# Kernel optimization log

Measured on AMD Instinct MI355X. Metric: run time of the kernel, lower is better.

Reference implementation:

```python
import jax, jax.numpy as jnp
import numpy as np

B, A, C, H, W = 8, 9, 21, 100, 100
M = 32
N = A * H * W
POS_THR, NEG_THR = 0.25, 0.1


def setup_inputs() -> dict:
    key = jax.random.key(0)
    k1, k2, k3, k4, k5, k6, k7 = jax.random.split(key, 7)
    cls_output = jax.random.normal(k1, (B, A, C, H, W), jnp.float32)
    reg_output = jax.random.normal(k2, (B, A, 4, H, W), jnp.float32) * 0.1
    # valid xyxy anchors: centers in [32,480], sizes in [16,128]
    ctr = jax.random.uniform(k3, (N, 2), minval=32.0, maxval=480.0)
    wh = jax.random.uniform(k4, (N, 2), minval=16.0, maxval=128.0)
    anchors = jnp.concatenate([ctr - wh / 2, ctr + wh / 2], axis=1)
    tctr = jax.random.uniform(k5, (B, M, 2), minval=32.0, maxval=480.0)
    twh = jax.random.uniform(k6, (B, M, 2), minval=16.0, maxval=128.0)
    target_boxes = jnp.concatenate([tctr - twh / 2, tctr + twh / 2], axis=2)
    target_labels = jax.random.randint(k7, (B, M), 1, C)
    return dict(cls_output=cls_output, reg_output=reg_output, anchors=anchors,
                target_boxes=target_boxes, target_labels=target_labels)


def _decode_boxes(reg, anchors):
    # inverse of the encode math in the loss: tx=(t*2-1), ctr=a_ctr+tx*aw/4, w=aw*exp(tw)
    aw = anchors[:, 2] - anchors[:, 0]
    ah = anchors[:, 3] - anchors[:, 1]
    acx = anchors[:, 0] + 0.5 * aw
    acy = anchors[:, 1] + 0.5 * ah
    tx = reg[:, 0] * 2.0 - 1.0
    ty = reg[:, 1] * 2.0 - 1.0
    cx = acx + tx * aw / 4.0
    cy = acy + ty * ah / 4.0
    w = aw * jnp.exp(reg[:, 2])
    h = ah * jnp.exp(reg[:, 3])
    return jnp.stack([cx - w / 2, cy - h / 2, cx + w / 2, cy + h / 2], axis=1)


def _pairwise_iou(a, b):  # a: [N,4], b: [M,4] xyxy
    lt = jnp.maximum(a[:, None, :2], b[None, :, :2])  # [N,M,2]
    rb = jnp.minimum(a[:, None, 2:], b[None, :, 2:])
    wh = jnp.clip(rb - lt, 0.0)
    inter = wh[..., 0] * wh[..., 1]
    area_a = (a[:, 2] - a[:, 0]) * (a[:, 3] - a[:, 1])
    area_b = (b[:, 2] - b[:, 0]) * (b[:, 3] - b[:, 1])
    union = area_a[:, None] + area_b[None, :] - inter
    return inter / jnp.maximum(union, 1e-8)


def _smooth_l1(d):
    ad = jnp.abs(d)
    return jnp.where(ad < 1.0, 0.5 * d * d, ad - 0.5)


def _per_image(cls_i, reg_i, anchors, boxes, labels):
    # [A,4,H,W] -> [4,A,H,W] -> [4,N] -> [N,4]; same for cls
    reg_flat = jnp.transpose(reg_i, (1, 0, 2, 3)).reshape(4, -1).T
    cls_flat = jnp.transpose(cls_i, (1, 0, 2, 3)).reshape(C, -1).T  # [N,C]
    decoded = _decode_boxes(reg_flat, anchors)
    ious = _pairwise_iou(decoded, boxes)  # [N,M]
    max_iou = ious.max(axis=1)
    max_idx = ious.argmax(axis=1)
    pos = max_iou >= POS_THR
    neg = max_iou < NEG_THR
    n_pos = pos.sum()
    n_neg = neg.sum()
    posf = pos.astype(cls_flat.dtype)
    negf = neg.astype(cls_flat.dtype)

    lse = jax.nn.logsumexp(cls_flat, axis=1)  # [N]
    matched_labels = labels[max_idx]  # [N]
    ce_pos = lse - jnp.take_along_axis(cls_flat, matched_labels[:, None], axis=1)[:, 0]
    ce_neg = lse - cls_flat[:, 0]
    cls_loss = (ce_pos * posf).sum() / jnp.maximum(n_pos, 1).astype(cls_flat.dtype)
    cls_loss = cls_loss + (ce_neg * negf).sum() / jnp.maximum(n_neg, 1).astype(cls_flat.dtype)

    # encode gt against anchors (vectorized over all N, masked to positives)
    aw = anchors[:, 2] - anchors[:, 0]
    ah = anchors[:, 3] - anchors[:, 1]
    acx = anchors[:, 0] + 0.5 * aw
    acy = anchors[:, 1] + 0.5 * ah
    gb = boxes[max_idx]  # [N,4]
    gw = gb[:, 2] - gb[:, 0]
    gh = gb[:, 3] - gb[:, 1]
    gcx = gb[:, 0] + 0.5 * gw
    gcy = gb[:, 1] + 0.5 * gh
    tx = ((gcx - acx) * (4.0 / aw) + 1.0) / 2.0
    ty = ((gcy - acy) * (4.0 / ah) + 1.0) / 2.0
    tw = jnp.log(gw / aw)
    th = jnp.log(gh / ah)
    reg_targets = jnp.stack([tx, ty, tw, th], axis=1)  # [N,4]
    sl1 = _smooth_l1(reg_flat - reg_targets)
    reg_loss = (sl1 * posf[:, None]).sum() / jnp.maximum(n_pos * 4, 1).astype(cls_flat.dtype)
    return cls_loss, reg_loss, n_pos


def reference(cls_output, reg_output, anchors, target_boxes, target_labels):
    cls_losses, reg_losses, n_pos = jax.vmap(
        _per_image, in_axes=(0, 0, None, 0, 0))(cls_output, reg_output, anchors,
                                                 target_boxes, target_labels)
    total_pos = n_pos.sum()
    cls_final = cls_losses.mean()
    reg_final = reg_losses.sum() / jnp.maximum(total_pos, 1).astype(cls_losses.dtype)
    total = cls_final + reg_final
    return total, cls_final, reg_final, total_pos
```

## Files before the change

### kernel.cpp

```cpp
#include <hip/hip_runtime.h>

#define HWSZ   10000
#define A_     9
#define C_     21
#define B_     8
#define M_     32
#define TPB    256
#define Q_     2500
#define SUBS   10
#define BPI    (A_*SUBS)
#define P_     (B_*BPI)

__device__ __forceinline__ float smooth_l1(float d) {
    float ad = fabsf(d);
    return ad < 1.f ? 0.5f * d * d : ad - 0.5f;
}

__device__ __forceinline__ float wave_red(float v) {
    #pragma unroll
    for (int o = 32; o; o >>= 1) v += __shfl_down(v, o);
    return v;
}

__device__ __forceinline__ float fc(const float4& v, int k) {
    return k == 0 ? v.x : k == 1 ? v.y : k == 2 ? v.z : v.w;
}

__device__ __forceinline__ void det_body(
    const float* __restrict__ cls, const float* __restrict__ reg,
    const float* __restrict__ anchors,
    const float4* sbox, const float* sarea, const int* slbl,
    int b, int a, int q,
    float& ce_pos, float& ce_neg, float& sl1, float& nposf, float& nnegf)
{
    float4 an[4], rg[4];
    const float4* anch4 = (const float4*)anchors + (size_t)a * HWSZ + q * 4;
    #pragma unroll
    for (int k = 0; k < 4; ++k) an[k] = anch4[k];
    const float4* reg4 = (const float4*)reg + ((b * A_ + a) * 4) * Q_ + q;
    #pragma unroll
    for (int k = 0; k < 4; ++k) rg[k] = reg4[k * Q_];
    const float4* cls4 = (const float4*)cls + ((b * A_ + a) * C_) * Q_ + q;
    float4 bufA[10];
    #pragma unroll
    for (int j = 0; j < 10; ++j) bufA[j] = cls4[j * Q_];

    float aw[4], ah[4], acx[4], acy[4];
    float r0[4], r1[4], r2[4], r3[4];
    float dx1[4], dy1[4], dx2[4], dy2[4], ara[4];
    #pragma unroll
    for (int k = 0; k < 4; ++k) {
        float4 A = an[k];
        aw[k] = A.z - A.x; ah[k] = A.w - A.y;
        acx[k] = A.x + 0.5f * aw[k]; acy[k] = A.y + 0.5f * ah[k];
        r0[k] = fc(rg[0], k); r1[k] = fc(rg[1], k);
        r2[k] = fc(rg[2], k); r3[k] = fc(rg[3], k);
        float tx = r0[k] * 2.f - 1.f, ty = r1[k] * 2.f - 1.f;
        float cx = acx[k] + tx * aw[k] * 0.25f;
        float cy = acy[k] + ty * ah[k] * 0.25f;
        float w = aw[k] * __expf(r2[k]), h = ah[k] * __expf(r3[k]);
        dx1[k] = cx - 0.5f * w; dy1[k] = cy - 0.5f * h;
        dx2[k] = cx + 0.5f * w; dy2[k] = cy + 0.5f * h;
        ara[k] = w * h;
    }

    float bi[4] = {-1.f, -1.f, -1.f, -1.f};
    float bu[4] = { 1.f,  1.f,  1.f,  1.f};
    int   bx_[4] = {0, 0, 0, 0};
    #pragma unroll 4
    for (int m = 0; m < M_; ++m) {
        float4 gb = sbox[m];
        float  am = sarea[m];
        #pragma unroll
        for (int k = 0; k < 4; ++k) {
            float lx = fmaxf(dx1[k], gb.x), ly = fmaxf(dy1[k], gb.y);
            float rx = fminf(dx2[k], gb.z), ry = fminf(dy2[k], gb.w);
            float iw = fmaxf(rx - lx, 0.f), ih = fmaxf(ry - ly, 0.f);
            float inter = iw * ih;
            float uni   = ara[k] + am - inter;
            bool  gt    = inter * bu[k] > bi[k] * uni;
            bi[k]  = gt ? inter : bi[k];
            bu[k]  = gt ? uni   : bu[k];
            bx_[k] = gt ? m     : bx_[k];
        }
    }

    float posf[4], negf[4];
    int   lbl[4];
    #pragma unroll
    for (int k = 0; k < 4; ++k) {
        posf[k] = (bi[k] >= 0.25f * bu[k]) ? 1.f : 0.f;
        negf[k] = (bi[k] <  0.10f * bu[k]) ? 1.f : 0.f;
        lbl[k]  = slbl[bx_[k]];
        float4 gb = sbox[bx_[k]];
        float gw = gb.z - gb.x, gh = gb.w - gb.y;
        float gcx = gb.x + 0.5f * gw, gcy = gb.y + 0.5f * gh;
        float raw = __builtin_amdgcn_rcpf(aw[k]);
        float rah = __builtin_amdgcn_rcpf(ah[k]);
        float ttx = ((gcx - acx[k]) * 4.f * raw + 1.f) * 0.5f;
        float tty = ((gcy - acy[k]) * 4.f * rah + 1.f) * 0.5f;
        float ttw = __logf(gw * raw), tth = __logf(gh * rah);
        float s4 = smooth_l1(r0[k] - ttx) + smooth_l1(r1[k] - tty)
                 + smooth_l1(r2[k] - ttw) + smooth_l1(r3[k] - tth);
        sl1   += s4 * posf[k];
        nposf += posf[k];
        nnegf += negf[k];
    }

    float4 bufB[11];
    #pragma unroll
    for (int j = 0; j < 11; ++j) bufB[j] = cls4[(10 + j) * Q_];

    float s[4], vlbl[4], v0[4];
    {
        float4 v = bufA[0];
        #pragma unroll
        for (int k = 0; k < 4; ++k) {
            float vk = fc(v, k);
            v0[k]   = vk;
            s[k]    = __expf(vk);
            vlbl[k] = (lbl[k] == 0) ? vk : 0.f;
        }
    }
    #pragma unroll
    for (int c = 1; c < 10; ++c) {
        float4 v = bufA[c];
        #pragma unroll
        for (int k = 0; k < 4; ++k) {
            float vk = fc(v, k);
            s[k] += __expf(vk);
            vlbl[k] = (lbl[k] == c) ? vk : vlbl[k];
        }
    }
    #pragma unroll
    for (int c = 10; c < C_; ++c) {
        float4 v = bufB[c - 10];
        #pragma unroll
        for (int k = 0; k < 4; ++k) {
            float vk = fc(v, k);
            s[k] += __expf(vk);
            vlbl[k] = (lbl[k] == c) ? vk : vlbl[k];
        }
    }
    #pragma unroll
    for (int k = 0; k < 4; ++k) {
        float lse = __logf(s[k]);
        ce_pos += (lse - vlbl[k]) * posf[k];
        ce_neg += (lse - v0[k])   * negf[k];
    }
}

__global__ __launch_bounds__(TPB, 3) void det_loss_main(
    const float* __restrict__ cls, const float* __restrict__ reg,
    const float* __restrict__ anchors, const float* __restrict__ tboxes,
    const int* __restrict__ tlabels, float* __restrict__ part)
{
    __shared__ float4 sbox[M_];
    __shared__ float  sarea[M_];
    __shared__ int    slbl[M_];
    __shared__ float  red[4][5];

    const int bid  = blockIdx.x;
    const int b    = bid & 7;
    const int rest = bid >> 3;
    const int a    = rest / SUBS;
    const int sub  = rest - a * SUBS;
    const int t    = threadIdx.x;

    if (t < M_) {
        float4 bx = ((const float4*)tboxes)[b * M_ + t];
        sbox[t]  = bx;
        sarea[t] = (bx.z - bx.x) * (bx.w - bx.y);
        slbl[t]  = tlabels[b * M_ + t];
    }
    __syncthreads();

    const int q = sub * TPB + t;
    float ce_pos = 0.f, ce_neg = 0.f, sl1 = 0.f, nposf = 0.f, nnegf = 0.f;
    if (q < Q_)
        det_body(cls, reg, anchors, sbox, sarea, slbl, b, a, q,
                 ce_pos, ce_neg, sl1, nposf, nnegf);

    ce_pos = wave_red(ce_pos);
    ce_neg = wave_red(ce_neg);
    sl1    = wave_red(sl1);
    nposf  = wave_red(nposf);
    nnegf  = wave_red(nnegf);

    const int wid = t >> 6, lane = t & 63;
    if (lane == 0) {
        red[wid][0] = ce_pos; red[wid][1] = ce_neg; red[wid][2] = sl1;
        red[wid][3] = nposf;  red[wid][4] = nnegf;
    }
    __syncthreads();
    if (t == 0) {
        float acc[5] = {0.f, 0.f, 0.f, 0.f, 0.f};
        #pragma unroll
        for (int wv = 0; wv < 4; ++wv)
            #pragma unroll
            for (int k = 0; k < 5; ++k) acc[k] += red[wv][k];
        const int p = b * BPI + rest;
        part[0 * P_ + p] = acc[0];
        part[1 * P_ + p] = acc[1];
        part[2 * P_ + p] = acc[2];
        part[3 * P_ + p] = acc[3];
        part[4 * P_ + p] = acc[4];
    }
}

__global__ __launch_bounds__(512) void det_loss_final(
    const float* __restrict__ part, float* __restrict__ out)
{
    __shared__ float res[B_][5];
    const int t = threadIdx.x;
    const int b = t >> 6, lane = t & 63;

    float a0 = 0.f, a1 = 0.f, a2 = 0.f, a3 = 0.f, a4 = 0.f;
    for (int p = lane; p < BPI; p += 64) {
        const int idx = b * BPI + p;
        a0 += part[0 * P_ + idx];
        a1 += part[1 * P_ + idx];
        a2 += part[2 * P_ + idx];
        a3 += part[3 * P_ + idx];
        a4 += part[4 * P_ + idx];
    }
    a0 = wave_red(a0); a1 = wave_red(a1); a2 = wave_red(a2);
    a3 = wave_red(a3); a4 = wave_red(a4);
    if (lane == 0) {
        res[b][0] = a0; res[b][1] = a1; res[b][2] = a2;
        res[b][3] = a3; res[b][4] = a4;
    }
    __syncthreads();
    if (t == 0) {
        float cls_sum = 0.f, reg_sum = 0.f, tp = 0.f;
        #pragma unroll
        for (int bb = 0; bb < B_; ++bb) {
            float cep = res[bb][0], cen = res[bb][1], sl = res[bb][2];
            float np  = res[bb][3], nn  = res[bb][4];
            cls_sum += cep / fmaxf(np, 1.f) + cen / fmaxf(nn, 1.f);
            reg_sum += sl / fmaxf(4.f * np, 1.f);
            tp += np;
        }
        float cls_final = cls_sum / (float)B_;
        float reg_final = reg_sum / fmaxf(tp, 1.f);
        out[0] = cls_final + reg_final;
        out[1] = cls_final;
        out[2] = reg_final;
        out[3] = tp;
    }
}

extern "C" void kernel_launch(void* const* d_in, const int* in_sizes, int n_in,
                              void* d_out, int out_size, void* d_ws, size_t ws_size,
                              hipStream_t stream) {
    const float* cls     = (const float*)d_in[0];
    const float* reg     = (const float*)d_in[1];
    const float* anchors = (const float*)d_in[2];
    const float* tboxes  = (const float*)d_in[3];
    const int*   tlabels = (const int*)d_in[4];
    float* part = (float*)d_ws;
    float* out  = (float*)d_out;

    det_loss_main<<<P_, TPB, 0, stream>>>(cls, reg, anchors, tboxes, tlabels, part);
    det_loss_final<<<1, 512, 0, stream>>>(part, out);
}
```

Baseline: 30.39 us.

## Fuse final reduction into main kernel via last-block atomic counter

Replaces the separate final-reduction kernel with a last-block-done pattern. Each block writes its partials with atomic stores and increments a global counter, and the block that sees the final count reduces all partials and writes the outputs. This removes the second kernel launch and its dependency gap, but adds a memset launch to reset the counter and an atomic on every block.

```diff
diff --git a/kernel.cpp b/kernel.cpp
--- a/kernel.cpp
+++ b/kernel.cpp
@@ -10,6 +10,8 @@
 #define SUBS   10
 #define BPI    (A_*SUBS)
 #define P_     (B_*BPI)
+#define SLOT   8
+#define CNT_OFF 32768
 
 __device__ __forceinline__ float smooth_l1(float d) {
     float ad = fabsf(d);
@@ -150,15 +152,18 @@
     }
 }
 
-__global__ __launch_bounds__(TPB, 3) void det_loss_main(
+__global__ __launch_bounds__(TPB, 3) void det_loss_fused(
     const float* __restrict__ cls, const float* __restrict__ reg,
     const float* __restrict__ anchors, const float* __restrict__ tboxes,
-    const int* __restrict__ tlabels, float* __restrict__ part)
+    const int* __restrict__ tlabels, float* __restrict__ part,
+    unsigned long long* __restrict__ cnt, float* __restrict__ out)
 {
     __shared__ float4 sbox[M_];
     __shared__ float  sarea[M_];
     __shared__ int    slbl[M_];
     __shared__ float  red[4][5];
+    __shared__ float  res[B_][5];
+    __shared__ int    lastflag;
 
     const int bid  = blockIdx.x;
     const int b    = bid & 7;
@@ -199,54 +204,58 @@
         for (int wv = 0; wv < 4; ++wv)
             #pragma unroll
             for (int k = 0; k < 5; ++k) acc[k] += red[wv][k];
-        const int p = b * BPI + rest;
-        part[0 * P_ + p] = acc[0];
-        part[1 * P_ + p] = acc[1];
-        part[2 * P_ + p] = acc[2];
-        part[3 * P_ + p] = acc[3];
-        part[4 * P_ + p] = acc[4];
-    }
-}
-
-__global__ __launch_bounds__(512) void det_loss_final(
-    const float* __restrict__ part, float* __restrict__ out)
-{
-    __shared__ float res[B_][5];
-    const int t = threadIdx.x;
-    const int b = t >> 6, lane = t & 63;
-
-    float a0 = 0.f, a1 = 0.f, a2 = 0.f, a3 = 0.f, a4 = 0.f;
-    for (int p = lane; p < BPI; p += 64) {
-        const int idx = b * BPI + p;
-        a0 += part[0 * P_ + idx];
-        a1 += part[1 * P_ + idx];
-        a2 += part[2 * P_ + idx];
-        a3 += part[3 * P_ + idx];
-        a4 += part[4 * P_ + idx];
-    }
-    a0 = wave_red(a0); a1 = wave_red(a1); a2 = wave_red(a2);
-    a3 = wave_red(a3); a4 = wave_red(a4);
-    if (lane == 0) {
-        res[b][0] = a0; res[b][1] = a1; res[b][2] = a2;
-        res[b][3] = a3; res[b][4] = a4;
+        #pragma unroll
+        for (int k = 0; k < 5; ++k)
+            __hip_atomic_store(&part[bid * SLOT + k], acc[k],
+                               __ATOMIC_RELAXED, __HIP_MEMORY_SCOPE_AGENT);
+        unsigned long long old = __hip_atomic_fetch_add(
+            cnt, 1ULL, __ATOMIC_ACQ_REL, __HIP_MEMORY_SCOPE_AGENT);
+        lastflag = (old == (unsigned long long)(P_ - 1)) ? 1 : 0;
     }
     __syncthreads();
-    if (t == 0) {
-        float cls_sum = 0.f, reg_sum = 0.f, tp = 0.f;
-        #pragma unroll
-        for (int bb = 0; bb < B_; ++bb) {
-            float cep = res[bb][0], cen = res[bb][1], sl = res[bb][2];
-            float np  = res[bb][3], nn  = res[bb][4];
-            cls_sum += cep / fmaxf(np, 1.f) + cen / fmaxf(nn, 1.f);
-            reg_sum += sl / fmaxf(4.f * np, 1.f);
-            tp += np;
-        }
-        float cls_final = cls_sum / (float)B_;
-        float reg_final = reg_sum / fmaxf(tp, 1.f);
-        out[0] = cls_final + reg_final;
-        out[1] = cls_final;
-        out[2] = reg_final;
-        out[3] = tp;
+
+    if (lastflag) {
+        const int img = t >> 5;
+        const int ln  = t & 31;
+        float a0 = 0.f, a1 = 0.f, a2 = 0.f, a3 = 0.f, a4 = 0.f;
+        for (int r = ln; r < BPI; r += 32) {
+            const float* sp = part + (size_t)(r * 8 + img) * SLOT;
+            a0 += __hip_atomic_load(sp + 0, __ATOMIC_RELAXED, __HIP_MEMORY_SCOPE_AGENT);
+            a1 += __hip_atomic_load(sp + 1, __ATOMIC_RELAXED, __HIP_MEMORY_SCOPE_AGENT);
+            a2 += __hip_atomic_load(sp + 2, __ATOMIC_RELAXED, __HIP_MEMORY_SCOPE_AGENT);
+            a3 += __hip_atomic_load(sp + 3, __ATOMIC_RELAXED, __HIP_MEMORY_SCOPE_AGENT);
+            a4 += __hip_atomic_load(sp + 4, __ATOMIC_RELAXED, __HIP_MEMORY_SCOPE_AGENT);
+        }
+        #pragma unroll
+        for (int o = 16; o; o >>= 1) {
+            a0 += __shfl_down(a0, o, 32);
+            a1 += __shfl_down(a1, o, 32);
+            a2 += __shfl_down(a2, o, 32);
+            a3 += __shfl_down(a3, o, 32);
+            a4 += __shfl_down(a4, o, 32);
+        }
+        if (ln == 0) {
+            res[img][0] = a0; res[img][1] = a1; res[img][2] = a2;
+            res[img][3] = a3; res[img][4] = a4;
+        }
+        __syncthreads();
+        if (t == 0) {
+            float cls_sum = 0.f, reg_sum = 0.f, tp = 0.f;
+            #pragma unroll
+            for (int bb = 0; bb < B_; ++bb) {
+                float cep = res[bb][0], cen = res[bb][1], sl = res[bb][2];
+                float np  = res[bb][3], nn  = res[bb][4];
+                cls_sum += cep / fmaxf(np, 1.f) + cen / fmaxf(nn, 1.f);
+                reg_sum += sl / fmaxf(4.f * np, 1.f);
+                tp += np;
+            }
+            float cls_final = cls_sum / (float)B_;
+            float reg_final = reg_sum / fmaxf(tp, 1.f);
+            out[0] = cls_final + reg_final;
+            out[1] = cls_final;
+            out[2] = reg_final;
+            out[3] = tp;
+        }
     }
 }
 
@@ -259,8 +268,11 @@
     const float* tboxes  = (const float*)d_in[3];
     const int*   tlabels = (const int*)d_in[4];
     float* part = (float*)d_ws;
+    unsigned long long* cnt =
+        (unsigned long long*)((char*)d_ws + CNT_OFF);
     float* out  = (float*)d_out;
 
-    det_loss_main<<<P_, TPB, 0, stream>>>(cls, reg, anchors, tboxes, tlabels, part);
-    det_loss_final<<<1, 512, 0, stream>>>(part, out);
-}
+    hipMemsetAsync(cnt, 0, sizeof(unsigned long long), stream);
+    det_loss_fused<<<P_, TPB, 0, stream>>>(
+        cls, reg, anchors, tboxes, tlabels, part, cnt, out);
+}
```

New measurement: 39.28 us. +29.3%, slower.
